# Kernel optimization log

Hardware: AMD Instinct MI355X
Metric: run time of the kernel (lower is better)

Reference implementation:

```python
import jax, jax.numpy as jnp
import numpy as np

K = 3    # kernel_size
PAD = 1  # (dilation*(K-1)+1)//2 with dilation=1
EPS = 1e-5


def _pad(x):
    # SAN pad_mode=1 -> reflection padding
    return jnp.pad(x, ((0, 0), (0, 0), (PAD, PAD), (PAD, PAD)), mode='reflect')


def _conv1x1(x, w, b=None):
    # x: (n, cin, H, W), w: (cout, cin)
    y = jnp.einsum('oc,nchw->nohw', w, x)
    if b is not None:
        y = y + b[None, :, None, None]
    return y


def _bn(x, g, b, m, v):
    # eval-mode BatchNorm over channel dim of (n, c, k, l)
    scale = g / jnp.sqrt(v + EPS)
    return (x - m[None, :, None, None]) * scale[None, :, None, None] + b[None, :, None, None]


def _position(H, W):
    loc_w = jnp.broadcast_to(jnp.linspace(-1.0, 1.0, W)[None, :], (H, W))
    loc_h = jnp.broadcast_to(jnp.linspace(-1.0, 1.0, H)[:, None], (H, W))
    return jnp.stack([loc_w, loc_h], 0)[None]  # (1, 2, H, W)


def setup_inputs() -> dict:
    key = jax.random.key(0)
    ks = jax.random.split(key, 32)
    n, cin, H, W = 16, 64, 256, 256
    rel, cout = 8, 64
    s = 0.05
    inp = {
        'x': jax.random.normal(ks[0], (n, cin, H, W), jnp.float32),
        'conv1_w': jax.random.normal(ks[1], (rel, cin), jnp.float32) * s,
        'conv1_b': jax.random.normal(ks[2], (rel,), jnp.float32) * s,
        'conv2_w': jax.random.normal(ks[3], (rel, cin), jnp.float32) * s,
        'conv2_b': jax.random.normal(ks[4], (rel,), jnp.float32) * s,
        'conv3_w': jax.random.normal(ks[5], (cout, cin), jnp.float32) * s,
        'conv3_b': jax.random.normal(ks[6], (cout,), jnp.float32) * s,
        'convp_w': jax.random.normal(ks[7], (2, 2), jnp.float32) * s,
        'convp_b': jax.random.normal(ks[8], (2,), jnp.float32) * s,
        'bn1_g': jax.random.uniform(ks[9], (rel + 2,), jnp.float32, 0.5, 1.5),
        'bn1_b': jax.random.normal(ks[10], (rel + 2,), jnp.float32) * s,
        'bn1_m': jax.random.normal(ks[11], (rel + 2,), jnp.float32) * s,
        'bn1_v': jax.random.uniform(ks[12], (rel + 2,), jnp.float32, 0.5, 1.5),
        'w_mid': jax.random.normal(ks[13], (rel, rel + 2), jnp.float32) * s,
        'bn2_g': jax.random.uniform(ks[14], (rel,), jnp.float32, 0.5, 1.5),
        'bn2_b': jax.random.normal(ks[15], (rel,), jnp.float32) * s,
        'bn2_m': jax.random.normal(ks[16], (rel,), jnp.float32) * s,
        'bn2_v': jax.random.uniform(ks[17], (rel,), jnp.float32, 0.5, 1.5),
        'w_out': jax.random.normal(ks[18], (1, rel), jnp.float32) * s,
        'b_out': jax.random.normal(ks[19], (1,), jnp.float32) * s,
    }
    return inp


def reference(x, conv1_w, conv1_b, conv2_w, conv2_b, conv3_w, conv3_b,
              convp_w, convp_b, bn1_g, bn1_b, bn1_m, bn1_v, w_mid,
              bn2_g, bn2_b, bn2_m, bn2_v, w_out, b_out):
    n, _, H, W = x.shape
    x1 = _conv1x1(x, conv1_w, conv1_b)   # (n, rel, H, W)
    x2 = _conv1x1(x, conv2_w, conv2_b)   # (n, rel, H, W)
    x3 = _conv1x1(x, conv3_w, conv3_b)   # (n, out, H, W)
    p = _conv1x1(_position(H, W), convp_w, convp_b)  # (1, 2, H, W)

    x2p, pp = _pad(x2), _pad(p)
    # Subtraction2: x1[center] - x2[neighbor]; Subtraction: p[center] - p[neighbor]
    d = jnp.stack([x1 - x2p[:, :, i:i + H, j:j + W]
                   for i in range(K) for j in range(K)], 2)  # (n, rel, 9, H, W)
    pd = jnp.stack([p - pp[:, :, i:i + H, j:j + W]
                    for i in range(K) for j in range(K)], 2)  # (1, 2, 9, H, W)
    rel = x1.shape[1]
    d = d.reshape(n, rel, K * K, H * W)
    pd = jnp.broadcast_to(pd.reshape(1, 2, K * K, H * W), (n, 2, K * K, H * W))
    feat = jnp.concatenate([d, pd], 1)  # (n, rel+2, 9, H*W)

    # conv_w1: BN -> ReLU -> 1x1 conv -> BN -> ReLU -> 1x1 conv
    h = jax.nn.relu(_bn(feat, bn1_g, bn1_b, bn1_m, bn1_v))
    h = jnp.einsum('oc,nckl->nokl', w_mid, h)
    h = jax.nn.relu(_bn(h, bn2_g, bn2_b, bn2_m, bn2_v))
    h = jnp.einsum('oc,nckl->nokl', w_out, h) + b_out[None, :, None, None]
    w = jax.nn.softmax(h, axis=-2)  # softmax over the k*k window axis
    w = w.reshape(n, 1, K * K, H, W)

    # Aggregation: weighted sum over the window (weight shared across channels)
    x3p = _pad(x3)
    out = jnp.zeros_like(x3)
    idx = 0
    for i in range(K):
        for j in range(K):
            out = out + w[:, :, idx] * x3p[:, :, i:i + H, j:j + W]
            idx += 1
    return out
```

## Files before the change

### kernel.cpp

```cpp
#include <hip/hip_runtime.h>
#include <stdint.h>

#define HH 256
#define WW 256
#define CIN 64
#define NPIX 65536
#define TW 64
#define TH 16
#define NCELL 1188
#define NCELLP 1216

typedef uint32_t u32;

__device__ __forceinline__ int refl(int t, int n) {
    if (t < 0) return -t;
    if (t >= n) return 2 * n - 2 - t;
    return t;
}

__device__ __forceinline__ void gload_lds4(const float* g, float* l) {
    __builtin_amdgcn_global_load_lds(
        (const __attribute__((address_space(1))) u32*)g,
        (__attribute__((address_space(3))) u32*)l, 4, 0, 0);
}

__device__ __forceinline__ u32 bfpack(float a, float b) {
    u32 ua = __float_as_uint(a), ub = __float_as_uint(b);
    ua = (ua + 0x7fffu + ((ua >> 16) & 1u)) >> 16;
    ub = (ub + 0x7fffu + ((ub >> 16) & 1u)) & 0xffff0000u;
    return ua | ub;
}
__device__ __forceinline__ float bflo(u32 v) { return __uint_as_float(v << 16); }
__device__ __forceinline__ float bfhi(u32 v) { return __uint_as_float(v & 0xffff0000u); }

__global__ __launch_bounds__(512, 4)
void san_weights(const float* __restrict__ x,
                 const float* __restrict__ w1, const float* __restrict__ b1,
                 const float* __restrict__ w2, const float* __restrict__ b2,
                 const float* __restrict__ cpw,
                 const float* __restrict__ bn1g, const float* __restrict__ bn1b,
                 const float* __restrict__ bn1m, const float* __restrict__ bn1v,
                 const float* __restrict__ wmid,
                 const float* __restrict__ bn2g, const float* __restrict__ bn2b,
                 const float* __restrict__ bn2m, const float* __restrict__ bn2v,
                 const float* __restrict__ wout, const float* __restrict__ bout,
                 float* __restrict__ w9)
{
    __shared__ float stage[8 * NCELLP];
    __shared__ uint4 x2l[NCELL];
    __shared__ uint4 x1l[TW * TH];

    const int n = blockIdx.z;
    const int ty = blockIdx.y * TH, tx = blockIdx.x * TW;
    const int tid = threadIdx.x;
    const int wave = tid >> 6, lane = tid & 63;
    const float* xn = x + (size_t)n * CIN * NPIX;

    float acc[3][16];
    #pragma unroll
    for (int o = 0; o < 8; ++o) {
        float b = b1[o];
        acc[0][o] = b; acc[1][o] = b; acc[2][o] = b;
    }
    #pragma unroll
    for (int o = 0; o < 8; ++o) {
        float b = b2[o];
        acc[0][8 + o] = b; acc[1][8 + o] = b; acc[2][8 + o] = b;
    }

    const int cA = tid, cB = tid + 512, cC = tid + 1024;
    const int cCc = (cC < NCELL) ? cC : 0;

    for (int c0 = 0; c0 < 64; c0 += 8) {
        if (c0) __syncthreads();
        for (int t = wave; t < 152; t += 8) {
            int cc = t / 19, r = t - cc * 19;
            int cell = r * 64 + lane;
            if (cell < NCELL) {
                int hy = cell / 66, hx = cell - hy * 66;
                int gy = refl(ty + hy - 1, HH), gx = refl(tx + hx - 1, WW);
                gload_lds4(xn + (size_t)(c0 + cc) * NPIX + gy * WW + gx,
                           &stage[cc * NCELLP + r * 64]);
            }
        }
        __syncthreads();

        float xv[3][8];
        #pragma unroll
        for (int j = 0; j < 8; ++j) {
            xv[0][j] = stage[j * NCELLP + cA];
            xv[1][j] = stage[j * NCELLP + cB];
            xv[2][j] = stage[j * NCELLP + cCc];
        }
        #pragma unroll
        for (int o = 0; o < 16; ++o) {
            const float* wr = (o < 8) ? (w1 + o * CIN + c0) : (w2 + (o - 8) * CIN + c0);
            #pragma unroll
            for (int j = 0; j < 8; ++j) {
                float wj = wr[j];
                acc[0][o] = fmaf(wj, xv[0][j], acc[0][o]);
                acc[1][o] = fmaf(wj, xv[1][j], acc[1][o]);
                acc[2][o] = fmaf(wj, xv[2][j], acc[2][o]);
            }
        }
    }

    #pragma unroll
    for (int ci = 0; ci < 3; ++ci) {
        int cell = tid + ci * 512;
        if (cell < NCELL) {
            uint4 v2;
            v2.x = bfpack(acc[ci][8],  acc[ci][9]);
            v2.y = bfpack(acc[ci][10], acc[ci][11]);
            v2.z = bfpack(acc[ci][12], acc[ci][13]);
            v2.w = bfpack(acc[ci][14], acc[ci][15]);
            x2l[cell] = v2;
            int hy = cell / 66, hx = cell - hy * 66;
            if (hy >= 1 && hy <= TH && hx >= 1 && hx <= TW) {
                uint4 v1;
                v1.x = bfpack(acc[ci][0], acc[ci][1]);
                v1.y = bfpack(acc[ci][2], acc[ci][3]);
                v1.z = bfpack(acc[ci][4], acc[ci][5]);
                v1.w = bfpack(acc[ci][6], acc[ci][7]);
                x1l[(hy - 1) * TW + (hx - 1)] = v1;
            }
        }
    }
    __syncthreads();

    float s1[10], o1[10];
    #pragma unroll
    for (int c = 0; c < 10; ++c) {
        float s = bn1g[c] * rsqrtf(bn1v[c] + 1e-5f);
        s1[c] = s;
        o1[c] = bn1b[c] - bn1m[c] * s;
    }
    float s2[8], o2[8];
    #pragma unroll
    for (int e = 0; e < 8; ++e) {
        float s = bn2g[e] * rsqrtf(bn2v[e] + 1e-5f);
        s2[e] = s;
        o2[e] = bn2b[e] - bn2m[e] * s;
    }
    const float cp00 = cpw[0], cp01 = cpw[1], cp10 = cpw[2], cp11 = cpw[3];
    const float bo = bout[0];

    #pragma unroll
    for (int pi = 0; pi < 2; ++pi) {
        int px = tid + pi * 512;
        int py = px >> 6, pxx = px & 63;
        int h = ty + py, w = tx + pxx;
        int cell = (py + 1) * 66 + (pxx + 1);
        uint4 v1 = x1l[px];
        float x1v[8];
        x1v[0] = bflo(v1.x); x1v[1] = bfhi(v1.x);
        x1v[2] = bflo(v1.y); x1v[3] = bfhi(v1.y);
        x1v[4] = bflo(v1.z); x1v[5] = bfhi(v1.z);
        x1v[6] = bflo(v1.w); x1v[7] = bfhi(v1.w);
        float lg[9];
        #pragma unroll
        for (int k = 0; k < 9; ++k) {
            int dy = k / 3 - 1, dx = k % 3 - 1;
            uint4 v2 = x2l[cell + dy * 66 + dx];
            float f[10];
            f[0] = x1v[0] - bflo(v2.x); f[1] = x1v[1] - bfhi(v2.x);
            f[2] = x1v[2] - bflo(v2.y); f[3] = x1v[3] - bfhi(v2.y);
            f[4] = x1v[4] - bflo(v2.z); f[5] = x1v[5] - bfhi(v2.z);
            f[6] = x1v[6] - bflo(v2.w); f[7] = x1v[7] - bfhi(v2.w);
            int hn = refl(h + dy, HH), wn = refl(w + dx, WW);
            float dp0 = (2.0f / 255.0f) * (float)(w - wn);
            float dp1 = (2.0f / 255.0f) * (float)(h - hn);
            f[8] = cp00 * dp0 + cp01 * dp1;
            f[9] = cp10 * dp0 + cp11 * dp1;
            float a[10];
            #pragma unroll
            for (int c = 0; c < 10; ++c)
                a[c] = fmaxf(fmaf(f[c], s1[c], o1[c]), 0.0f);
            float lgk = bo;
            #pragma unroll
            for (int e = 0; e < 8; ++e) {
                float g = 0.0f;
                #pragma unroll
                for (int c = 0; c < 10; ++c) g = fmaf(wmid[e * 10 + c], a[c], g);
                g = fmaxf(fmaf(g, s2[e], o2[e]), 0.0f);
                lgk = fmaf(wout[e], g, lgk);
            }
            lg[k] = lgk;
        }
        float m = lg[0];
        #pragma unroll
        for (int k = 1; k < 9; ++k) m = fmaxf(m, lg[k]);
        float e9[9], ssum = 0.0f;
        #pragma unroll
        for (int k = 0; k < 9; ++k) { e9[k] = __expf(lg[k] - m); ssum += e9[k]; }
        float inv = 1.0f / ssum;
        size_t base = (size_t)n * 9 * NPIX + (size_t)h * WW + w;
        #pragma unroll
        for (int k = 0; k < 9; ++k) w9[base + (size_t)k * NPIX] = e9[k] * inv;
    }
}

__global__ __launch_bounds__(1024, 4)
void san_agg(const float* __restrict__ x, const float* __restrict__ w9,
             const float* __restrict__ w3, const float* __restrict__ b3,
             float* __restrict__ out)
{
    __shared__ float buf[2][16 * NCELLP];
    const int n = blockIdx.z;
    const int ty = blockIdx.y * TH, tx = blockIdx.x * TW;
    const int tid = threadIdx.x;
    const int wave = tid >> 6, lane = tid & 63;
    const int pxx = tid & 63, py = tid >> 6;
    const int h = ty + py, w = tx + pxx;
    const float* xn = x + (size_t)n * CIN * NPIX;

    float wk[9];
    {
        size_t wb = (size_t)n * 9 * NPIX + (size_t)h * WW + w;
        #pragma unroll
        for (int k = 0; k < 9; ++k) wk[k] = w9[wb + (size_t)k * NPIX];
    }
    float acc[64];
    #pragma unroll
    for (int o = 0; o < 64; ++o) acc[o] = 0.0f;

    const int cellc = (py + 1) * 66 + (pxx + 1);

    auto stage = [&](int ch0, int b) {
        for (int t = wave; t < 304; t += 16) {
            int cc = t / 19, r = t - cc * 19;
            int cell = r * 64 + lane;
            if (cell < NCELL) {
                int hy = cell / 66, hx = cell - hy * 66;
                int gy = refl(ty + hy - 1, HH), gx = refl(tx + hx - 1, WW);
                gload_lds4(xn + (size_t)(ch0 + cc) * NPIX + gy * WW + gx,
                           &buf[b][cc * NCELLP + r * 64]);
            }
        }
    };

    stage(0, 0);
    for (int kc = 0; kc < 4; ++kc) {
        __syncthreads();
        if (kc < 3) stage((kc + 1) * 16, (kc + 1) & 1);
        const float* bp = buf[kc & 1];
        float sv[16];
        #pragma unroll
        for (int cc = 0; cc < 16; ++cc) {
            const float* p = bp + cc * NCELLP + cellc;
            float s = wk[0] * p[-67];
            s = fmaf(wk[1], p[-66], s);
            s = fmaf(wk[2], p[-65], s);
            s = fmaf(wk[3], p[-1],  s);
            s = fmaf(wk[4], p[0],   s);
            s = fmaf(wk[5], p[1],   s);
            s = fmaf(wk[6], p[65],  s);
            s = fmaf(wk[7], p[66],  s);
            s = fmaf(wk[8], p[67],  s);
            sv[cc] = s;
        }
        const int c0 = kc * 16;
        #pragma unroll
        for (int o = 0; o < 64; ++o) {
            const float* wr = w3 + o * CIN + c0;
            #pragma unroll
            for (int cc = 0; cc < 16; ++cc)
                acc[o] = fmaf(wr[cc], sv[cc], acc[o]);
        }
    }
    size_t ob = (size_t)n * CIN * NPIX + (size_t)h * WW + w;
    #pragma unroll
    for (int o = 0; o < 64; ++o)
        out[ob + (size_t)o * NPIX] = acc[o] + b3[o];
}

extern "C" void kernel_launch(void* const* d_in, const int* in_sizes, int n_in,
                              void* d_out, int out_size, void* d_ws, size_t ws_size,
                              hipStream_t stream) {
    const float* x      = (const float*)d_in[0];
    const float* w1     = (const float*)d_in[1];
    const float* b1     = (const float*)d_in[2];
    const float* w2     = (const float*)d_in[3];
    const float* b2     = (const float*)d_in[4];
    const float* w3     = (const float*)d_in[5];
    const float* b3     = (const float*)d_in[6];
    const float* cpw    = (const float*)d_in[7];
    const float* bn1g   = (const float*)d_in[9];
    const float* bn1b   = (const float*)d_in[10];
    const float* bn1m   = (const float*)d_in[11];
    const float* bn1v   = (const float*)d_in[12];
    const float* wmid   = (const float*)d_in[13];
    const float* bn2g   = (const float*)d_in[14];
    const float* bn2b   = (const float*)d_in[15];
    const float* bn2m   = (const float*)d_in[16];
    const float* bn2v   = (const float*)d_in[17];
    const float* wout   = (const float*)d_in[18];
    const float* bout   = (const float*)d_in[19];
    float* out = (float*)d_out;
    float* w9  = (float*)d_ws;

    dim3 grid(WW / TW, HH / TH, 16);
    san_weights<<<grid, 512, 0, stream>>>(x, w1, b1, w2, b2, cpw,
                                          bn1g, bn1b, bn1m, bn1v, wmid,
                                          bn2g, bn2b, bn2m, bn2v, wout, bout, w9);
    san_agg<<<grid, 1024, 0, stream>>>(x, w9, w3, b3, out);
}
```

Measured before the change: 798.9 us.

## Use bf16 MFMA with split-precision operands for the aggregation 1x1 conv

The per-pixel 64x64 channel-mixing FMA loop in san_agg is replaced by MFMA 16x16x32 bf16 instructions. Weights and aggregated activations are split into high and low bf16 parts to keep near-fp32 accuracy. Pixels are remapped per wave so each lane computes aggregated values for matrix fragments, with shuffles building the B operands. Bias is folded into the accumulator init and the LDS row stride changes. The goal is to offload the dominant FP32 FMA work to matrix cores, at the cost of extra pack, shuffle and MFMA passes and some precision risk.

```diff
diff --git a/kernel.cpp b/kernel.cpp
--- a/kernel.cpp
+++ b/kernel.cpp
@@ -9,8 +9,13 @@
 #define TH 16
 #define NCELL 1188
 #define NCELLP 1216
+#define NCELLP2 1196
 
 typedef uint32_t u32;
+typedef __attribute__((ext_vector_type(4))) float f32x4;
+typedef __attribute__((ext_vector_type(8))) short short8;
+
+union FR { u32 u[4]; short8 s; };
 
 __device__ __forceinline__ int refl(int t, int n) {
     if (t < 0) return -t;
@@ -32,6 +37,13 @@
 }
 __device__ __forceinline__ float bflo(u32 v) { return __uint_as_float(v << 16); }
 __device__ __forceinline__ float bfhi(u32 v) { return __uint_as_float(v & 0xffff0000u); }
+
+__device__ __forceinline__ u32 pack2t(float a, float b) {
+    return (__float_as_uint(a) >> 16) | (__float_as_uint(b) & 0xffff0000u);
+}
+__device__ __forceinline__ float bftrunc(float a) {
+    return __uint_as_float(__float_as_uint(a) & 0xffff0000u);
+}
 
 __global__ __launch_bounds__(512, 4)
 void san_weights(const float* __restrict__ x,
@@ -205,26 +217,17 @@
              const float* __restrict__ w3, const float* __restrict__ b3,
              float* __restrict__ out)
 {
-    __shared__ float buf[2][16 * NCELLP];
-    const int n = blockIdx.z;
+    __shared__ float buf[2][16 * NCELLP2];
+    __shared__ u32 whf[4][4][128];
+
+    const int nb = blockIdx.z;
     const int ty = blockIdx.y * TH, tx = blockIdx.x * TW;
     const int tid = threadIdx.x;
     const int wave = tid >> 6, lane = tid & 63;
-    const int pxx = tid & 63, py = tid >> 6;
-    const int h = ty + py, w = tx + pxx;
-    const float* xn = x + (size_t)n * CIN * NPIX;
-
-    float wk[9];
-    {
-        size_t wb = (size_t)n * 9 * NPIX + (size_t)h * WW + w;
-        #pragma unroll
-        for (int k = 0; k < 9; ++k) wk[k] = w9[wb + (size_t)k * NPIX];
-    }
-    float acc[64];
-    #pragma unroll
-    for (int o = 0; o < 64; ++o) acc[o] = 0.0f;
-
-    const int cellc = (py + 1) * 66 + (pxx + 1);
+    const int q = lane >> 4, nn = lane & 15;
+    const int oct = q & 1;
+    const int half = lane >> 5;
+    const float* xn = x + (size_t)nb * CIN * NPIX;
 
     auto stage = [&](int ch0, int b) {
         for (int t = wave; t < 304; t += 16) {
@@ -234,44 +237,127 @@
                 int hy = cell / 66, hx = cell - hy * 66;
                 int gy = refl(ty + hy - 1, HH), gx = refl(tx + hx - 1, WW);
                 gload_lds4(xn + (size_t)(ch0 + cc) * NPIX + gy * WW + gx,
-                           &buf[b][cc * NCELLP + r * 64]);
+                           &buf[b][cc * NCELLP2 + r * 64]);
             }
         }
     };
 
     stage(0, 0);
+
+    {
+        int t = tid;
+        int kcp = t >> 8, mtp = (t >> 6) & 3, l2 = (t >> 1) & 31, rp = (t & 1) * 2;
+        int m = mtp * 16 + (l2 & 15);
+        int col = kcp * 16 + (l2 >> 4) * 8 + rp * 2;
+        const float* wr = w3 + m * 64 + col;
+        whf[kcp][mtp][l2 * 4 + rp]     = pack2t(wr[0], wr[1]);
+        whf[kcp][mtp][l2 * 4 + rp + 1] = pack2t(wr[2], wr[3]);
+    }
+
+    float wk2[2][9];
+    int cellc[2];
+    {
+        const int h = ty + wave;
+        #pragma unroll
+        for (int s = 0; s < 2; ++s) {
+            int xw = (2 * s + half) * 16 + nn;
+            cellc[s] = (wave + 1) * 66 + xw + 1;
+            size_t wb = (size_t)nb * 9 * NPIX + (size_t)h * WW + (tx + xw);
+            #pragma unroll
+            for (int k = 0; k < 9; ++k) wk2[s][k] = w9[wb + (size_t)k * NPIX];
+        }
+    }
+
+    f32x4 acc[4][4];
+    #pragma unroll
+    for (int mt = 0; mt < 4; ++mt) {
+        #pragma unroll
+        for (int j = 0; j < 4; ++j) {
+            float bv = b3[mt * 16 + q * 4 + j];
+            acc[mt][0][j] = bv; acc[mt][1][j] = bv;
+            acc[mt][2][j] = bv; acc[mt][3][j] = bv;
+        }
+    }
+
+    __syncthreads();
+
     for (int kc = 0; kc < 4; ++kc) {
-        __syncthreads();
         if (kc < 3) stage((kc + 1) * 16, (kc + 1) & 1);
         const float* bp = buf[kc & 1];
-        float sv[16];
-        #pragma unroll
-        for (int cc = 0; cc < 16; ++cc) {
-            const float* p = bp + cc * NCELLP + cellc;
-            float s = wk[0] * p[-67];
-            s = fmaf(wk[1], p[-66], s);
-            s = fmaf(wk[2], p[-65], s);
-            s = fmaf(wk[3], p[-1],  s);
-            s = fmaf(wk[4], p[0],   s);
-            s = fmaf(wk[5], p[1],   s);
-            s = fmaf(wk[6], p[65],  s);
-            s = fmaf(wk[7], p[66],  s);
-            s = fmaf(wk[8], p[67],  s);
-            sv[cc] = s;
-        }
-        const int c0 = kc * 16;
-        #pragma unroll
-        for (int o = 0; o < 64; ++o) {
-            const float* wr = w3 + o * CIN + c0;
-            #pragma unroll
-            for (int cc = 0; cc < 16; ++cc)
-                acc[o] = fmaf(wr[cc], sv[cc], acc[o]);
-        }
-    }
-    size_t ob = (size_t)n * CIN * NPIX + (size_t)h * WW + w;
-    #pragma unroll
-    for (int o = 0; o < 64; ++o)
-        out[ob + (size_t)o * NPIX] = acc[o] + b3[o];
+
+        u32 frag[4][4];
+        #pragma unroll
+        for (int s = 0; s < 2; ++s) {
+            const float* cb = bp + oct * 8 * NCELLP2 + cellc[s];
+            float sv[8];
+            #pragma unroll
+            for (int j = 0; j < 8; ++j) {
+                const float* p = cb + j * NCELLP2;
+                float t = wk2[s][0] * p[-67];
+                t = fmaf(wk2[s][1], p[-66], t);
+                t = fmaf(wk2[s][2], p[-65], t);
+                t = fmaf(wk2[s][3], p[-1],  t);
+                t = fmaf(wk2[s][4], p[0],   t);
+                t = fmaf(wk2[s][5], p[1],   t);
+                t = fmaf(wk2[s][6], p[65],  t);
+                t = fmaf(wk2[s][7], p[66],  t);
+                t = fmaf(wk2[s][8], p[67],  t);
+                sv[j] = t;
+            }
+            #pragma unroll
+            for (int r = 0; r < 4; ++r) {
+                float a = sv[2 * r], b = sv[2 * r + 1];
+                u32 sh = pack2t(a, b);
+                u32 sl = pack2t(a - bftrunc(a), b - bftrunc(b));
+                u32 shx = __shfl_xor(sh, 32);
+                u32 slx = __shfl_xor(sl, 32);
+                frag[2 * s + 0][r] = (half == 0) ? sh  : slx;
+                frag[2 * s + 1][r] = (half == 0) ? shx : sl;
+            }
+        }
+
+        #pragma unroll
+        for (int mt = 0; mt < 4; ++mt) {
+            FR wh, wl;
+            #pragma unroll
+            for (int r = 0; r < 4; ++r) wh.u[r] = whf[kc][mt][(lane & 31) * 4 + r];
+            const float* wrow = w3 + (mt * 16 + nn) * 64 + kc * 16 + oct * 8;
+            #pragma unroll
+            for (int r = 0; r < 4; ++r) {
+                float a = wrow[2 * r], b = wrow[2 * r + 1];
+                wl.u[r] = pack2t(a - bftrunc(a), b - bftrunc(b));
+            }
+            #pragma unroll
+            for (int pg = 0; pg < 4; ++pg) {
+                FR bf;
+                bf.u[0] = frag[pg][0]; bf.u[1] = frag[pg][1];
+                bf.u[2] = frag[pg][2]; bf.u[3] = frag[pg][3];
+                acc[mt][pg] = __builtin_amdgcn_mfma_f32_16x16x32_bf16(
+                    wh.s, bf.s, acc[mt][pg], 0, 0, 0);
+                acc[mt][pg] = __builtin_amdgcn_mfma_f32_16x16x32_bf16(
+                    wl.s, bf.s, acc[mt][pg], 0, 0, 0);
+            }
+        }
+
+        if (kc < 3) __syncthreads();
+    }
+
+    {
+        const int h = ty + wave;
+        size_t ob = (size_t)nb * CIN * NPIX + (size_t)h * WW + tx;
+        #pragma unroll
+        for (int mt = 0; mt < 4; ++mt) {
+            #pragma unroll
+            for (int pg = 0; pg < 4; ++pg) {
+                size_t pb = ob + (size_t)pg * 16 + nn;
+                #pragma unroll
+                for (int j = 0; j < 4; ++j) {
+                    int m = mt * 16 + q * 4 + j;
+                    out[pb + (size_t)m * NPIX] = acc[mt][pg][j];
+                }
+            }
+        }
+    }
 }
 
 extern "C" void kernel_launch(void* const* d_in, const int* in_sizes, int n_in,
```

Result: slower. 994.7 us (+24.5%).
